# Optimization experiments

Hardware: AMD Instinct MI355X
Metric: run time of the kernel (lower is better)

The kernel has to match this reference:

```python
import jax, jax.numpy as jnp
import numpy as np

VOC_SIZE = 512
CHAR_EMB = 128
N_FILT = 16
KERNELS = [2, 3, 4, 5, 6]
PADS = [0, 0, 1, 2, 3]
B, L = 16384, 32


def _conv1d(x, w, b, pad):
    # x: [B, C, L], w: [O, I, K] -> [B, O, L_out]
    y = jax.lax.conv_general_dilated(
        x, w, window_strides=(1,), padding=[(pad, pad)],
        dimension_numbers=("NCH", "OIH", "NCH"))
    return y + b[None, :, None]


def setup_inputs() -> dict:
    key = jax.random.key(0)
    ks = jax.random.split(key, 12)
    word = jax.random.randint(ks[0], (B, L), 0, VOC_SIZE, dtype=jnp.int64 if jax.config.jax_enable_x64 else jnp.int32)
    emb = jax.random.normal(ks[1], (VOC_SIZE, CHAR_EMB), dtype=jnp.float32) * 0.1
    inp = {"word": word, "emb": emb}
    for i, k in enumerate(KERNELS):
        fan_in = CHAR_EMB * k
        bound = 1.0 / np.sqrt(fan_in)
        inp[f"w{k}"] = jax.random.uniform(ks[2 + 2 * i], (N_FILT, CHAR_EMB, k), jnp.float32, -bound, bound)
        inp[f"b{k}"] = jax.random.uniform(ks[3 + 2 * i], (N_FILT,), jnp.float32, -bound, bound)
    return inp


def reference(word, emb, w2, b2, w3, b3, w4, b4, w5, b5, w6, b6):
    unk = word < 0                      # [B, L]
    idx = jnp.where(unk, 0, word)
    x = emb[idx]                        # [B, L, E]
    x = jnp.where(unk[..., None], 0.0, x)
    x = jnp.transpose(x, (0, 2, 1))     # [B, E, L]
    ws = [w2, w3, w4, w5, w6]
    bs = [b2, b3, b4, b5, b6]
    maxima = [jnp.max(_conv1d(x, w, b, p), axis=-1)
              for w, b, p in zip(ws, bs, PADS)]  # each [B, 16]
    return jnp.concatenate(maxima, axis=-1)      # [B, 80]
```

## Files before the change

kernel.cpp:

```cpp
#include <hip/hip_runtime.h>
#include <hip/hip_fp16.h>
#include <math.h>

#define VOC      512
#define EMB      128
#define L_SEQ    32
#define NWORDS   16384
#define NCOL     416
#define WPB      128
#define SCPITCH  129

__device__ __constant__ int SEGBASE_H[5] = {0, 16416, 49248, 82080, 147744};
__device__ __constant__ int SEGW_H[5]    = {32, 64, 64, 128, 128};

__global__ __launch_bounds__(NCOL) void pack_wt(
    const float* __restrict__ w2, const float* __restrict__ w3,
    const float* __restrict__ w4, const float* __restrict__ w5,
    const float* __restrict__ w6,
    float* __restrict__ wt)
{
    const int i   = blockIdx.x;
    const int col = threadIdx.x;

    int k, jpad, base; const float* w;
    if (col < 32)       { k = 2; jpad = 2; base = 0;   w = w2; }
    else if (col < 96)  { k = 3; jpad = 4; base = 32;  w = w3; }
    else if (col < 160) { k = 4; jpad = 4; base = 96;  w = w4; }
    else if (col < 288) { k = 5; jpad = 8; base = 160; w = w5; }
    else                { k = 6; jpad = 8; base = 288; w = w6; }

    const int r  = col - base;
    const int ol = (jpad == 2) ? (r >> 1) : (jpad == 4) ? (r >> 2) : (r >> 3);
    const int j  = r & (jpad - 1);

    wt[i * NCOL + col] = (j < k) ? w[(ol * EMB + i) * k + j] : 0.f;
}

__device__ __forceinline__ void col_map(int col, int& seg, int& local) {
    if (col < 32)       { seg = 0; local = col; }
    else if (col < 96)  { seg = 1; local = col - 32; }
    else if (col < 160) { seg = 2; local = col - 96; }
    else if (col < 288) { seg = 3; local = col - 160; }
    else                { seg = 4; local = col - 288; }
}

__global__ __launch_bounds__(512) void build_pe16(
    const float* __restrict__ emb,
    const float* __restrict__ wt,
    __half* __restrict__ pe)
{
    const int c   = blockIdx.x;
    const int tid = threadIdx.x;

    if (c == VOC) {
        if (tid < NCOL) {
            int seg, local; col_map(tid, seg, local);
            pe[SEGBASE_H[seg] + VOC * SEGW_H[seg] + local] = __float2half(0.f);
        }
        return;
    }

    __shared__ float e[EMB];
    if (tid < EMB) e[tid] = emb[c * EMB + tid];
    __syncthreads();
    if (tid >= NCOL) return;

    float s = 0.f;
    #pragma unroll 8
    for (int i = 0; i < EMB; ++i) s += e[i] * wt[i * NCOL + tid];

    int seg, local; col_map(tid, seg, local);
    pe[SEGBASE_H[seg] + c * SEGW_H[seg] + local] = __float2half(s);
}

__device__ __forceinline__ float2 h2tof2(int u) {
    return __half22float2(__builtin_bit_cast(__half2, u));
}

template<int K> struct LdT;
template<> struct LdT<2> { using T = int;  };
template<> struct LdT<3> { using T = int2; };
template<> struct LdT<4> { using T = int2; };
template<> struct LdT<5> { using T = int4; };
template<> struct LdT<6> { using T = int4; };

template<int K>
__device__ __forceinline__ void unpack(typename LdT<K>::T q, float* v) {
    if constexpr (K == 2) {
        float2 f = h2tof2(q); v[0] = f.x; v[1] = f.y;
    } else if constexpr (K == 3) {
        float2 f0 = h2tof2(q.x), f1 = h2tof2(q.y);
        v[0] = f0.x; v[1] = f0.y; v[2] = f1.x;
    } else if constexpr (K == 4) {
        float2 f0 = h2tof2(q.x), f1 = h2tof2(q.y);
        v[0] = f0.x; v[1] = f0.y; v[2] = f1.x; v[3] = f1.y;
    } else if constexpr (K == 5) {
        float2 f0 = h2tof2(q.x), f1 = h2tof2(q.y), f2 = h2tof2(q.z);
        v[0] = f0.x; v[1] = f0.y; v[2] = f1.x; v[3] = f1.y; v[4] = f2.x;
    } else {
        float2 f0 = h2tof2(q.x), f1 = h2tof2(q.y), f2 = h2tof2(q.z);
        v[0] = f0.x; v[1] = f0.y; v[2] = f1.x; v[3] = f1.y;
        v[4] = f2.x; v[5] = f2.y;
    }
}

template<int K, int PAD, int LANEB>
__device__ __forceinline__ float convseg(const char* __restrict__ tab,
                                         const int* __restrict__ sc,
                                         int w, int ol, float bias)
{
    using LT = typename LdT<K>::T;
    constexpr int LOUT = L_SEQ + 2 * PAD - K + 1;
    const int lb = ol * LANEB;

    float s[LOUT];
    #pragma unroll
    for (int t = 0; t < LOUT; ++t) s[t] = bias;

    #pragma unroll
    for (int g = 0; g < 4; ++g) {
        int off[8];
        #pragma unroll
        for (int u = 0; u < 8; ++u)
            off[u] = sc[(g * 8 + u) * SCPITCH + w] + lb;
        LT q[8];
        #pragma unroll
        for (int u = 0; u < 8; ++u)
            q[u] = *(const LT*)(tab + off[u]);
        #pragma unroll
        for (int u = 0; u < 8; ++u) {
            const int tp = g * 8 + u;
            float v[K];
            unpack<K>(q[u], v);
            #pragma unroll
            for (int j = 0; j < K; ++j) {
                int t = tp + PAD - j;
                if (t >= 0 && t < LOUT) s[t] += v[j];
            }
        }
    }

    float m = s[0];
    #pragma unroll
    for (int t = 1; t < LOUT; ++t) m = fmaxf(m, s[t]);
    return m;
}

__global__ __launch_bounds__(1024) void conv_max(
    const int*    __restrict__ word,
    const __half* __restrict__ pe,
    const float* __restrict__ b2, const float* __restrict__ b3,
    const float* __restrict__ b4, const float* __restrict__ b5,
    const float* __restrict__ b6,
    float*       __restrict__ out)
{
    __shared__ __align__(16) __half tab[65664];
    __shared__ int sc[L_SEQ * SCPITCH];

    const int tid   = threadIdx.x;
    const int seg   = blockIdx.x % 5;
    const int wb    = blockIdx.x / 5;
    const int wbase = wb * WPB;

    const int segwH = SEGW_H[seg];
    const int nI4   = (513 * segwH) >> 3;

    const int4* src = (const int4*)(pe + SEGBASE_H[seg]);
    int4* dst = (int4*)tab;
    for (int i = tid; i < nI4; i += 1024) dst[i] = src[i];

    const int segwB = segwH * 2;
    #pragma unroll
    for (int r = 0; r < 4; ++r) {
        int i = tid + r * 1024;
        int c = word[wbase * L_SEQ + i];
        int w = i >> 5, tp = i & 31;
        sc[tp * SCPITCH + w] = (c >= 0 ? c : VOC) * segwB;
    }
    __syncthreads();

    const int ol = tid & 15;
    const int w0 = tid >> 4;
    const float* bp;
    switch (seg) {
        case 0:  bp = b2; break; case 1: bp = b3; break;
        case 2:  bp = b4; break; case 3: bp = b5; break;
        default: bp = b6; break;
    }
    const float bias = bp[ol];
    const char* tb = (const char*)tab;

    float m0, m1;
    switch (seg) {
        case 0:  m0 = convseg<2, 0, 4 >(tb, sc, w0,      ol, bias);
                 m1 = convseg<2, 0, 4 >(tb, sc, w0 + 64, ol, bias); break;
        case 1:  m0 = convseg<3, 0, 8 >(tb, sc, w0,      ol, bias);
                 m1 = convseg<3, 0, 8 >(tb, sc, w0 + 64, ol, bias); break;
        case 2:  m0 = convseg<4, 1, 8 >(tb, sc, w0,      ol, bias);
                 m1 = convseg<4, 1, 8 >(tb, sc, w0 + 64, ol, bias); break;
        case 3:  m0 = convseg<5, 2, 16>(tb, sc, w0,      ol, bias);
                 m1 = convseg<5, 2, 16>(tb, sc, w0 + 64, ol, bias); break;
        default: m0 = convseg<6, 3, 16>(tb, sc, w0,      ol, bias);
                 m1 = convseg<6, 3, 16>(tb, sc, w0 + 64, ol, bias); break;
    }
    out[(wbase + w0     ) * 80 + seg * 16 + ol] = m0;
    out[(wbase + w0 + 64) * 80 + seg * 16 + ol] = m1;
}

extern "C" void kernel_launch(void* const* d_in, const int* in_sizes, int n_in,
                              void* d_out, int out_size, void* d_ws, size_t ws_size,
                              hipStream_t stream)
{
    const int*   word = (const int*)  d_in[0];
    const float* emb  = (const float*)d_in[1];
    const float* w2   = (const float*)d_in[2];
    const float* b2   = (const float*)d_in[3];
    const float* w3   = (const float*)d_in[4];
    const float* b3   = (const float*)d_in[5];
    const float* w4   = (const float*)d_in[6];
    const float* b4   = (const float*)d_in[7];
    const float* w5   = (const float*)d_in[8];
    const float* b5   = (const float*)d_in[9];
    const float* w6   = (const float*)d_in[10];
    const float* b6   = (const float*)d_in[11];
    float* out = (float*)d_out;

    __half* pe16 = (__half*)d_ws;
    float*  wt   = (float*)((char*)d_ws + 430080);

    pack_wt<<<EMB, NCOL, 0, stream>>>(w2, w3, w4, w5, w6, wt);

    build_pe16<<<VOC + 1, 512, 0, stream>>>(emb, wt, pe16);

    conv_max<<<5 * (NWORDS / WPB), 1024, 0, stream>>>(
        word, pe16, b2, b3, b4, b5, b6, out);
}
```

Measured before the change: 106.7 us.

## Split conv blocks by filter half, shrink LDS table and use rolling conv window

The conv kernel now launches ten block types per word tile, one per (kernel size, half of the filters). Each block copies only half of the precomputed projection table into LDS, and it stores token indices as ushort with shift-based offsets. Each thread handles one word instead of two and keeps a K-wide rolling accumulator that folds into a running max, rather than a full per-position sum array, with launch_bounds raised for occupancy. build_pe16 now processes four vocab rows per block and the zero row for unknown tokens is written in LDS. The costs are more blocks, each reloading its own table half, and more complex indexing.

```diff
diff --git a/kernel.cpp b/kernel.cpp
--- a/kernel.cpp
+++ b/kernel.cpp
@@ -8,10 +8,11 @@
 #define NWORDS   16384
 #define NCOL     416
 #define WPB      128
-#define SCPITCH  129
-
-__device__ __constant__ int SEGBASE_H[5] = {0, 16416, 49248, 82080, 147744};
+#define SCP      130
+
+__device__ __constant__ int SEGBASE_H[5] = {0, 16384, 49152, 81920, 147456};
 __device__ __constant__ int SEGW_H[5]    = {32, 64, 64, 128, 128};
+__device__ __constant__ int CCSHIFT[5]   = {1, 2, 2, 3, 3};
 
 __global__ __launch_bounds__(NCOL) void pack_wt(
     const float* __restrict__ w2, const float* __restrict__ w3,
@@ -49,28 +50,27 @@
     const float* __restrict__ wt,
     __half* __restrict__ pe)
 {
-    const int c   = blockIdx.x;
+    const int c0  = blockIdx.x * 4;
     const int tid = threadIdx.x;
 
-    if (c == VOC) {
-        if (tid < NCOL) {
-            int seg, local; col_map(tid, seg, local);
-            pe[SEGBASE_H[seg] + VOC * SEGW_H[seg] + local] = __float2half(0.f);
-        }
-        return;
-    }
-
-    __shared__ float e[EMB];
-    if (tid < EMB) e[tid] = emb[c * EMB + tid];
+    __shared__ float e[4][EMB];
+    e[tid >> 7][tid & 127] = emb[c0 * EMB + tid];
     __syncthreads();
     if (tid >= NCOL) return;
 
-    float s = 0.f;
+    float s[4] = {0.f, 0.f, 0.f, 0.f};
     #pragma unroll 8
-    for (int i = 0; i < EMB; ++i) s += e[i] * wt[i * NCOL + tid];
+    for (int i = 0; i < EMB; ++i) {
+        float wv = wt[i * NCOL + tid];
+        #pragma unroll
+        for (int wc = 0; wc < 4; ++wc) s[wc] += e[wc][i] * wv;
+    }
 
     int seg, local; col_map(tid, seg, local);
-    pe[SEGBASE_H[seg] + c * SEGW_H[seg] + local] = __float2half(s);
+    const int base = SEGBASE_H[seg], segw = SEGW_H[seg];
+    #pragma unroll
+    for (int wc = 0; wc < 4; ++wc)
+        pe[base + (c0 + wc) * segw + local] = __float2half(s[wc]);
 }
 
 __device__ __forceinline__ float2 h2tof2(int u) {
@@ -104,25 +104,26 @@
     }
 }
 
-template<int K, int PAD, int LANEB>
+template<int K, int PAD, int SHIFT, int JPADB>
 __device__ __forceinline__ float convseg(const char* __restrict__ tab,
-                                         const int* __restrict__ sc,
-                                         int w, int ol, float bias)
+                                         const ushort* __restrict__ sc,
+                                         int w, int ol8, float bias)
 {
     using LT = typename LdT<K>::T;
     constexpr int LOUT = L_SEQ + 2 * PAD - K + 1;
-    const int lb = ol * LANEB;
-
-    float s[LOUT];
-    #pragma unroll
-    for (int t = 0; t < LOUT; ++t) s[t] = bias;
+    const int lb = ol8 * JPADB;
+
+    float win[K];
+    #pragma unroll
+    for (int i = 0; i < K; ++i) win[i] = bias;
+    float m = -INFINITY;
 
     #pragma unroll
     for (int g = 0; g < 4; ++g) {
         int off[8];
         #pragma unroll
         for (int u = 0; u < 8; ++u)
-            off[u] = sc[(g * 8 + u) * SCPITCH + w] + lb;
+            off[u] = ((int)sc[(g * 8 + u) * SCP + w] << SHIFT) + lb;
         LT q[8];
         #pragma unroll
         for (int u = 0; u < 8; ++u)
@@ -132,21 +133,24 @@
             const int tp = g * 8 + u;
             float v[K];
             unpack<K>(q[u], v);
+            const int topen = tp + PAD;
+            if (topen >= K && topen < LOUT) win[topen % K] = bias;
             #pragma unroll
             for (int j = 0; j < K; ++j) {
                 int t = tp + PAD - j;
-                if (t >= 0 && t < LOUT) s[t] += v[j];
+                if (t >= 0 && t < LOUT) win[t % K] += v[j];
             }
+            const int tcl = tp + PAD - (K - 1);
+            if (tcl >= 0) m = fmaxf(m, win[((unsigned)tcl) % K]);
         }
     }
-
-    float m = s[0];
-    #pragma unroll
-    for (int t = 1; t < LOUT; ++t) m = fmaxf(m, s[t]);
+    #pragma unroll
+    for (int t = L_SEQ + PAD - K + 1; t < LOUT; ++t)
+        m = fmaxf(m, win[((unsigned)t) % K]);
     return m;
 }
 
-__global__ __launch_bounds__(1024) void conv_max(
+__global__ __launch_bounds__(1024, 8) void conv_max(
     const int*    __restrict__ word,
     const __half* __restrict__ pe,
     const float* __restrict__ b2, const float* __restrict__ b3,
@@ -154,57 +158,56 @@
     const float* __restrict__ b6,
     float*       __restrict__ out)
 {
-    __shared__ __align__(16) __half tab[65664];
-    __shared__ int sc[L_SEQ * SCPITCH];
-
-    const int tid   = threadIdx.x;
-    const int seg   = blockIdx.x % 5;
-    const int wb    = blockIdx.x / 5;
-    const int wbase = wb * WPB;
-
-    const int segwH = SEGW_H[seg];
-    const int nI4   = (513 * segwH) >> 3;
-
-    const int4* src = (const int4*)(pe + SEGBASE_H[seg]);
-    int4* dst = (int4*)tab;
-    for (int i = tid; i < nI4; i += 1024) dst[i] = src[i];
-
-    const int segwB = segwH * 2;
+    __shared__ __align__(16) int4 tab4[513 * 8];
+    __shared__ ushort sc[L_SEQ * SCP];
+
+    const int tid  = threadIdx.x;
+    const int type = blockIdx.x % 10;
+    const int tile = blockIdx.x / 10;
+    const int seg  = type >> 1;
+    const int oh   = type & 1;
+
+    const int cc     = 1 << CCSHIFT[seg];
+    const int ccsh   = CCSHIFT[seg];
+    const int halfB  = cc << 4;
+    const int base_b = SEGBASE_H[seg] * 2 + oh * halfB;
+    const char* peb  = (const char*)pe;
+
+    for (int i = tid; i < (512 << ccsh); i += 1024)
+        tab4[i] = *(const int4*)(peb + base_b
+                                 + ((i >> ccsh) << (ccsh + 5))
+                                 + ((i & (cc - 1)) << 4));
+    if (tid < cc) tab4[(512 << ccsh) + tid] = int4{0, 0, 0, 0};
+
+    const int wbase = tile * WPB;
     #pragma unroll
     for (int r = 0; r < 4; ++r) {
         int i = tid + r * 1024;
         int c = word[wbase * L_SEQ + i];
-        int w = i >> 5, tp = i & 31;
-        sc[tp * SCPITCH + w] = (c >= 0 ? c : VOC) * segwB;
+        sc[(i & 31) * SCP + (i >> 5)] = (ushort)(c >= 0 ? c : VOC);
     }
     __syncthreads();
 
-    const int ol = tid & 15;
-    const int w0 = tid >> 4;
+    const int ol8 = tid & 7;
+    const int w   = tid >> 3;
     const float* bp;
     switch (seg) {
         case 0:  bp = b2; break; case 1: bp = b3; break;
         case 2:  bp = b4; break; case 3: bp = b5; break;
         default: bp = b6; break;
     }
-    const float bias = bp[ol];
-    const char* tb = (const char*)tab;
-
-    float m0, m1;
+    const float bias = bp[oh * 8 + ol8];
+    const char* tb = (const char*)tab4;
+
+    float m;
     switch (seg) {
-        case 0:  m0 = convseg<2, 0, 4 >(tb, sc, w0,      ol, bias);
-                 m1 = convseg<2, 0, 4 >(tb, sc, w0 + 64, ol, bias); break;
-        case 1:  m0 = convseg<3, 0, 8 >(tb, sc, w0,      ol, bias);
-                 m1 = convseg<3, 0, 8 >(tb, sc, w0 + 64, ol, bias); break;
-        case 2:  m0 = convseg<4, 1, 8 >(tb, sc, w0,      ol, bias);
-                 m1 = convseg<4, 1, 8 >(tb, sc, w0 + 64, ol, bias); break;
-        case 3:  m0 = convseg<5, 2, 16>(tb, sc, w0,      ol, bias);
-                 m1 = convseg<5, 2, 16>(tb, sc, w0 + 64, ol, bias); break;
-        default: m0 = convseg<6, 3, 16>(tb, sc, w0,      ol, bias);
-                 m1 = convseg<6, 3, 16>(tb, sc, w0 + 64, ol, bias); break;
-    }
-    out[(wbase + w0     ) * 80 + seg * 16 + ol] = m0;
-    out[(wbase + w0 + 64) * 80 + seg * 16 + ol] = m1;
+        case 0:  m = convseg<2, 0, 5, 4 >(tb, sc, w, ol8, bias); break;
+        case 1:  m = convseg<3, 0, 6, 8 >(tb, sc, w, ol8, bias); break;
+        case 2:  m = convseg<4, 1, 6, 8 >(tb, sc, w, ol8, bias); break;
+        case 3:  m = convseg<5, 2, 7, 16>(tb, sc, w, ol8, bias); break;
+        default: m = convseg<6, 3, 7, 16>(tb, sc, w, ol8, bias); break;
+    }
+    out[(wbase + w) * 80 + (seg << 4) + (oh << 3) + ol8] = m;
 }
 
 extern "C" void kernel_launch(void* const* d_in, const int* in_sizes, int n_in,
@@ -230,8 +233,8 @@
 
     pack_wt<<<EMB, NCOL, 0, stream>>>(w2, w3, w4, w5, w6, wt);
 
-    build_pe16<<<VOC + 1, 512, 0, stream>>>(emb, wt, pe16);
-
-    conv_max<<<5 * (NWORDS / WPB), 1024, 0, stream>>>(
+    build_pe16<<<VOC / 4, 512, 0, stream>>>(emb, wt, pe16);
+
+    conv_max<<<10 * (NWORDS / WPB), 1024, 0, stream>>>(
         word, pe16, b2, b3, b4, b5, b6, out);
 }
```

After: 111.3 us. 4.3% more time.
